# Optimization experiments

Measured on AMD Instinct MI355X. Metric: run time of the kernel, lower is better.

## Reference

```python
import jax, jax.numpy as jnp
import numpy as np
from jax import lax

B, C, N = 2048, 16, 32
POOL, STRIDE = 4, 2  # MaxPool2d(4, stride=2) -> output dim (N-4)//2+1 = 15


def setup_inputs() -> dict:
    key = jax.random.key(0)
    a = jax.random.normal(key, (B, C, N, N), dtype=jnp.float32)
    # Make each matrix symmetric positive definite: (A A^T)/N + I
    x = jnp.matmul(a, jnp.swapaxes(a, -1, -2)) / N + jnp.eye(N, dtype=jnp.float32)
    return {"x": x}


def _sym_fn(m, fn):
    """Apply fn to eigenvalues of batched symmetric matrices m and reconstruct."""
    w, v = jnp.linalg.eigh(m)                      # w: [..., n], v: [..., n, n]
    return jnp.matmul(v * fn(w)[..., None, :], jnp.swapaxes(v, -1, -2))


def reference(x):
    # LogEig: U log(S) U^T
    log_x = _sym_fn(x, jnp.log)                    # [B, C, N, N]
    # MaxPool2d(4, stride=2) over the last two dims
    pooled = lax.reduce_window(
        log_x,
        -jnp.inf,
        lax.max,
        window_dimensions=(1, 1, POOL, POOL),
        window_strides=(1, 1, STRIDE, STRIDE),
        padding="VALID",
    )                                              # [B, C, 15, 15] (still symmetric)
    # ExpEig: U exp(S) U^T
    return _sym_fn(pooled, jnp.exp)
```

## Files before the change

kernel.cpp:

```cpp
#include <hip/hip_runtime.h>
#include <cmath>


#define CENTER 4.5f
#define INVH   0.2857142857142857f
#define LDH 40
#define LDW 36
#define LDE 20

struct LogCoeffs { float b[16]; };

typedef __attribute__((ext_vector_type(8))) short bf16x8_t;
typedef __attribute__((ext_vector_type(4))) float f32x4_t;

#define MFMA_B16 __builtin_amdgcn_mfma_f32_16x16x32_bf16

__device__ __forceinline__ short bf16rne(float x) {
  unsigned u = __float_as_uint(x);
  unsigned r = (u + 0x7FFFu + ((u >> 16) & 1u)) >> 16;
  return (short)r;
}
__device__ __forceinline__ float bf16tof(short h) {
  return __uint_as_float(((unsigned)(unsigned short)h) << 16);
}

__device__ __forceinline__ void mprod(const short* Ah, const short* Al,
                                      const short* Bh, const short* Bl,
                                      f32x4_t acc[2][2], int r15, int k0) {
  const bf16x8_t a0h = *(const bf16x8_t*)(Ah + r15*LDH + k0);
  const bf16x8_t a1h = *(const bf16x8_t*)(Ah + (16 + r15)*LDH + k0);
  const bf16x8_t a0l = *(const bf16x8_t*)(Al + r15*LDH + k0);
  const bf16x8_t a1l = *(const bf16x8_t*)(Al + (16 + r15)*LDH + k0);
  const bf16x8_t b0h = *(const bf16x8_t*)(Bh + r15*LDH + k0);
  const bf16x8_t b1h = *(const bf16x8_t*)(Bh + (16 + r15)*LDH + k0);
  const bf16x8_t b0l = *(const bf16x8_t*)(Bl + r15*LDH + k0);
  const bf16x8_t b1l = *(const bf16x8_t*)(Bl + (16 + r15)*LDH + k0);
  acc[0][0] = MFMA_B16(a0h, b0h, acc[0][0], 0, 0, 0);
  acc[0][0] = MFMA_B16(a0h, b0l, acc[0][0], 0, 0, 0);
  acc[0][0] = MFMA_B16(a0l, b0h, acc[0][0], 0, 0, 0);
  acc[0][1] = MFMA_B16(a0h, b1h, acc[0][1], 0, 0, 0);
  acc[0][1] = MFMA_B16(a0h, b1l, acc[0][1], 0, 0, 0);
  acc[0][1] = MFMA_B16(a0l, b1h, acc[0][1], 0, 0, 0);
  acc[1][0] = MFMA_B16(a1h, b0h, acc[1][0], 0, 0, 0);
  acc[1][0] = MFMA_B16(a1h, b0l, acc[1][0], 0, 0, 0);
  acc[1][0] = MFMA_B16(a1l, b0h, acc[1][0], 0, 0, 0);
  acc[1][1] = MFMA_B16(a1h, b1h, acc[1][1], 0, 0, 0);
  acc[1][1] = MFMA_B16(a1h, b1l, acc[1][1], 0, 0, 0);
  acc[1][1] = MFMA_B16(a1l, b1h, acc[1][1], 0, 0, 0);
}

__device__ __forceinline__ void epi_hl(short* Dh, short* Dl,
                                       const f32x4_t acc[2][2], int r15, int quad) {
#pragma unroll
  for (int I = 0; I < 2; ++I)
#pragma unroll
    for (int i = 0; i < 4; ++i) {
      const int row = 16*I + quad + i;
#pragma unroll
      for (int J = 0; J < 2; ++J) {
        const float v = acc[I][J][i];
        const short h = bf16rne(v);
        const short lo = bf16rne(v - bf16tof(h));
        Dh[row*LDH + 16*J + r15] = h;
        Dl[row*LDH + 16*J + r15] = lo;
      }
    }
}

__device__ __forceinline__ void combo(f32x4_t c[2][2], float k0c, float k1c, float k2c,
                                      const f32x4_t Tt[2][2], const f32x4_t T2t[2][2],
                                      int r15, int quad) {
#pragma unroll
  for (int I = 0; I < 2; ++I)
#pragma unroll
    for (int J = 0; J < 2; ++J)
#pragma unroll
      for (int i = 0; i < 4; ++i) {
        float v = fmaf(k2c, T2t[I][J][i], k1c * Tt[I][J][i]);
        if (I == J && (quad + i) == r15) v += k0c;
        c[I][J][i] = v;
      }
}

__device__ __forceinline__ void mm16(const float* __restrict__ P,
                                     const float* __restrict__ Q,
                                     float a[4], int r, int c) {
  const float* p = P + r*LDE;
  const float* q = Q + 4*c;
#pragma unroll 4
  for (int k = 0; k < 4; ++k) {
    const float4 pv = *(const float4*)(p + 4*k);
    const float pr[4] = {pv.x, pv.y, pv.z, pv.w};
#pragma unroll
    for (int jj = 0; jj < 4; ++jj) {
      const float4 qv = *(const float4*)(q + (4*k + jj)*LDE);
      a[0] = fmaf(pr[jj], qv.x, a[0]);
      a[1] = fmaf(pr[jj], qv.y, a[1]);
      a[2] = fmaf(pr[jj], qv.z, a[2]);
      a[3] = fmaf(pr[jj], qv.w, a[3]);
    }
  }
}

__global__ __launch_bounds__(64, 4)
void logeig_pool_expeig(const float* __restrict__ x, float* __restrict__ out,
                        LogCoeffs lc) {
  __shared__ __align__(16) float S[2560];
  short* S0h = (short*)(S);            short* S0l = S0h + 1280;
  short* S1h = (short*)(S + 1280);     short* S1l = S1h + 1280;
  float* W   = S;
  float* RM  = S + 1280;
  float* E   = S + 1280;

  const int m = blockIdx.x;
  const int t = threadIdx.x;
  const int r15 = t & 15;
  const int k0 = (t >> 4) * 8;
  const int quad = (t >> 4) * 4;
  const float* xg = x + (size_t)m * 1024;


#pragma unroll
  for (int i = 0; i < 4; ++i) {
    int fi = (i*64 + t) * 4;
    float4 v = *(const float4*)(xg + fi);
    int row = fi >> 5, cb = fi & 31, dpos = row - cb;
    float* vp = (float*)&v;
    short hs[4], ls[4];
#pragma unroll
    for (int e = 0; e < 4; ++e) {
      float val = vp[e];
      if (e == dpos) val -= CENTER;
      val *= INVH;
      short h = bf16rne(val);
      hs[e] = h;
      ls[e] = bf16rne(val - bf16tof(h));
    }
    *(short4*)(S0h + row*LDH + cb) = make_short4(hs[0], hs[1], hs[2], hs[3]);
    *(short4*)(S0l + row*LDH + cb) = make_short4(ls[0], ls[1], ls[2], ls[3]);
  }

  f32x4_t Tt[2][2];
#pragma unroll
  for (int I = 0; I < 2; ++I)
#pragma unroll
    for (int J = 0; J < 2; ++J)
#pragma unroll
      for (int i = 0; i < 4; ++i) {
        const int row = 16*I + quad + i, col = 16*J + r15;
        Tt[I][J][i] = bf16tof(S0h[row*LDH + col]) + bf16tof(S0l[row*LDH + col]);
      }

  f32x4_t acc[2][2];
#pragma unroll
  for (int I = 0; I < 2; ++I)
#pragma unroll
    for (int J = 0; J < 2; ++J)
#pragma unroll
      for (int i = 0; i < 4; ++i) acc[I][J][i] = 0.0f;

  mprod(S0h, S0l, S0h, S0l, acc, r15, k0);
  f32x4_t T2t[2][2];
#pragma unroll
  for (int I = 0; I < 2; ++I)
#pragma unroll
    for (int J = 0; J < 2; ++J) T2t[I][J] = acc[I][J];
  epi_hl(S1h, S1l, acc, r15, quad);

#pragma unroll
  for (int I = 0; I < 2; ++I)
#pragma unroll
    for (int J = 0; J < 2; ++J)
#pragma unroll
      for (int i = 0; i < 4; ++i) acc[I][J][i] = 0.0f;
  mprod(S1h, S1l, S0h, S0l, acc, r15, k0);
  epi_hl(S0h, S0l, acc, r15, quad);

  {
    f32x4_t cc[2][2];
    combo(cc, lc.b[9], lc.b[10], lc.b[11], Tt, T2t, r15, quad);
    epi_hl(S1h, S1l, cc, r15, quad);
  }

  combo(acc, lc.b[6], lc.b[7], lc.b[8], Tt, T2t, r15, quad);
  mprod(S1h, S1l, S0h, S0l, acc, r15, k0);
  epi_hl(S1h, S1l, acc, r15, quad);

  combo(acc, lc.b[3], lc.b[4], lc.b[5], Tt, T2t, r15, quad);
  mprod(S1h, S1l, S0h, S0l, acc, r15, k0);
  epi_hl(S1h, S1l, acc, r15, quad);

  combo(acc, lc.b[0], lc.b[1], lc.b[2], Tt, T2t, r15, quad);
  mprod(S1h, S1l, S0h, S0l, acc, r15, k0);
#pragma unroll
  for (int I = 0; I < 2; ++I)
#pragma unroll
    for (int i = 0; i < 4; ++i) {
      const int row = 16*I + quad + i;
#pragma unroll
      for (int J = 0; J < 2; ++J)
        W[row*LDW + 16*J + r15] = acc[I][J][i];
    }

  {
    const int half = t >> 5, l = t & 31;
    const float* rp = W + l*LDW + 16*half;
    float4 w0 = *(const float4*)(rp + 0);
    float4 w1 = *(const float4*)(rp + 4);
    float4 w2 = *(const float4*)(rp + 8);
    float4 w3 = *(const float4*)(rp + 12);
    float2 e2 = *(const float2*)(W + l*LDW + 16);
    float v[16] = {w0.x,w0.y,w0.z,w0.w, w1.x,w1.y,w1.z,w1.w,
                   w2.x,w2.y,w2.z,w2.w, w3.x,w3.y,w3.z,w3.w};
    float rm[8];
#pragma unroll
    for (int j = 0; j < 7; ++j)
      rm[j] = fmaxf(fmaxf(v[2*j], v[2*j+1]), fmaxf(v[2*j+2], v[2*j+3]));
    rm[7] = (half == 0) ? fmaxf(fmaxf(v[14], v[15]), fmaxf(e2.x, e2.y)) : 0.0f;
    *(float4*)(RM + l*16 + 8*half + 0) = make_float4(rm[0], rm[1], rm[2], rm[3]);
    *(float4*)(RM + l*16 + 8*half + 4) = make_float4(rm[4], rm[5], rm[6], rm[7]);
  }

  const int r16 = t >> 2, c16 = t & 3;
  float p16[4];
  if (r16 < 15) {
    float4 m0 = *(const float4*)(RM + (2*r16 + 0)*16 + 4*c16);
    float4 m1 = *(const float4*)(RM + (2*r16 + 1)*16 + 4*c16);
    float4 m2 = *(const float4*)(RM + (2*r16 + 2)*16 + 4*c16);
    float4 m3 = *(const float4*)(RM + (2*r16 + 3)*16 + 4*c16);
    p16[0] = fmaxf(fmaxf(m0.x, m1.x), fmaxf(m2.x, m3.x));
    p16[1] = fmaxf(fmaxf(m0.y, m1.y), fmaxf(m2.y, m3.y));
    p16[2] = fmaxf(fmaxf(m0.z, m1.z), fmaxf(m2.z, m3.z));
    p16[3] = fmaxf(fmaxf(m0.w, m1.w), fmaxf(m2.w, m3.w));
    if (c16 == 3) p16[3] = 0.0f;
  } else {
    p16[0] = p16[1] = p16[2] = p16[3] = 0.0f;
  }

  float s = fabsf(p16[0]) + fabsf(p16[1]) + fabsf(p16[2]) + fabsf(p16[3]);
  s += __shfl_xor(s, 1);
  s += __shfl_xor(s, 2);
  s = fmaxf(s, __shfl_xor(s, 4));
  s = fmaxf(s, __shfl_xor(s, 8));
  s = fmaxf(s, __shfl_xor(s, 16));
  s = fmaxf(s, __shfl_xor(s, 32));
  int e2i; (void)frexpf(s, &e2i);
  const int sc = e2i > 0 ? e2i : 0;
  const float scale = ldexpf(1.0f, -sc);

  float* Te  = E;
  float* T2e = E + 320;
  float* T3e = E + 640;
  float* Me  = E + 960;

  float Tet[4] = {p16[0]*scale, p16[1]*scale, p16[2]*scale, p16[3]*scale};
  *(float4*)(Te + r16*LDE + 4*c16) = make_float4(Tet[0], Tet[1], Tet[2], Tet[3]);

  const float C0_ = 1.0f, C1_ = 1.0f, C2_ = 0.5f;
  const float C3_ = 1.6666667e-1f, C4_ = 4.1666668e-2f, C5_ = 8.3333338e-3f;
  const float C6_ = 1.3888889e-3f, C7_ = 1.9841270e-4f, C8_ = 2.4801588e-5f;

  float a4[4];
  a4[0] = a4[1] = a4[2] = a4[3] = 0.0f;
  mm16(Te, Te, a4, r16, c16);
  float T2et[4] = {a4[0], a4[1], a4[2], a4[3]};
  *(float4*)(T2e + r16*LDE + 4*c16) = make_float4(a4[0], a4[1], a4[2], a4[3]);
  a4[0] = a4[1] = a4[2] = a4[3] = 0.0f;
  mm16(T2e, Te, a4, r16, c16);
  *(float4*)(T3e + r16*LDE + 4*c16) = make_float4(a4[0], a4[1], a4[2], a4[3]);
#pragma unroll
  for (int e = 0; e < 4; ++e) {
    float v = fmaf(C8_, T2et[e], C7_ * Tet[e]);
    if (4*c16 + e == r16) v += C6_;
    a4[e] = v;
  }
  *(float4*)(Me + r16*LDE + 4*c16) = make_float4(a4[0], a4[1], a4[2], a4[3]);
#pragma unroll
  for (int e = 0; e < 4; ++e) {
    float v = fmaf(C5_, T2et[e], C4_ * Tet[e]);
    if (4*c16 + e == r16) v += C3_;
    a4[e] = v;
  }
  mm16(Me, T3e, a4, r16, c16);
  *(float4*)(T2e + r16*LDE + 4*c16) = make_float4(a4[0], a4[1], a4[2], a4[3]);
#pragma unroll
  for (int e = 0; e < 4; ++e) {
    float v = fmaf(C2_, T2et[e], C1_ * Tet[e]);
    if (4*c16 + e == r16) v += C0_;
    a4[e] = v;
  }
  mm16(T2e, T3e, a4, r16, c16);
  *(float4*)(Te + r16*LDE + 4*c16) = make_float4(a4[0], a4[1], a4[2], a4[3]);

  float* pc = Te;
  float* po = T3e;
  for (int it = 0; it < sc; ++it) {
    a4[0] = a4[1] = a4[2] = a4[3] = 0.0f;
    mm16(pc, pc, a4, r16, c16);
    *(float4*)(po + r16*LDE + 4*c16) = make_float4(a4[0], a4[1], a4[2], a4[3]);
    float* tmp = pc; pc = po; po = tmp;
  }

  float* og = out + (size_t)m * 225;
#pragma unroll
  for (int w2 = 0; w2 < 4; ++w2) {
    int q = t + 64*w2;
    if (q < 225) {
      int i = q / 15, j = q % 15;
      og[q] = pc[i*LDE + j];
    }
  }
}

extern "C" void kernel_launch(void* const* d_in, const int* in_sizes, int n_in,
                              void* d_out, int out_size, void* d_ws, size_t ws_size,
                              hipStream_t stream) {
  (void)n_in; (void)d_ws; (void)ws_size; (void)out_size;
  const float* x = (const float*)d_in[0];
  float* out = (float*)d_out;
  const int nmat = in_sizes[0] >> 10;

  LogCoeffs lc;
  {
    const double lo = 1.0, hi = 8.0;
    const double c = 0.5*(lo + hi), h = 0.5*(hi - lo), w = h / c;
    const double z = (std::sqrt(1.0 - w*w) - 1.0) / w;
    const int DEG = 11;
    double a[16] = {0};
    a[0] = std::log(c) - std::log(1.0 + z*z);
    double zk = 1.0;
    for (int k = 1; k <= DEG; ++k) { zk *= z; a[k] = -2.0 * zk / k; }
    double b[16], Tp[16], Tc[16], Tn[16];
    for (int j = 0; j < 16; ++j) { b[j] = 0; Tp[j] = 0; Tc[j] = 0; }
    Tp[0] = 1.0; Tc[1] = 1.0;
    b[0] += a[0] * Tp[0];
    for (int j = 0; j < 16; ++j) b[j] += a[1] * Tc[j];
    for (int k = 2; k <= DEG; ++k) {
      for (int j = 0; j < 16; ++j) {
        double v = -Tp[j];
        if (j > 0) v += 2.0 * Tc[j-1];
        Tn[j] = v;
      }
      for (int j = 0; j < 16; ++j) b[j] += a[k] * Tn[j];
      for (int j = 0; j < 16; ++j) { Tp[j] = Tc[j]; Tc[j] = Tn[j]; }
    }
    for (int j = 0; j < 16; ++j) lc.b[j] = (float)b[j];
  }

  logeig_pool_expeig<<<dim3(nmat), dim3(64), 0, stream>>>(x, out, lc);
}
```

Before: 258.5 us.

## Move 16x16 exp-stage matrix products to bf16 split MFMA and transpose epilogues

Replaces the scalar FP32 16x16 matrix products of the exp polynomial and squaring loop with bf16 hi/lo split MFMA instructions. Operands are stored packed as hi|lo halves in one row. The 32x32 log-stage epilogues now write transposed short4 vectors, relying on symmetry, instead of scattered scalar stores. This cuts FMA-pipe and LDS traffic in the exp stage, but it adds bf16 rounding on every matrix product and relies on the operands staying symmetric.

```diff
diff --git a/kernel.cpp b/kernel.cpp
--- a/kernel.cpp
+++ b/kernel.cpp
@@ -6,7 +6,6 @@
 #define INVH   0.2857142857142857f
 #define LDH 40
 #define LDW 36
-#define LDE 20
 
 struct LogCoeffs { float b[16]; };
 
@@ -49,21 +48,22 @@
   acc[1][1] = MFMA_B16(a1l, b1h, acc[1][1], 0, 0, 0);
 }
 
-__device__ __forceinline__ void epi_hl(short* Dh, short* Dl,
-                                       const f32x4_t acc[2][2], int r15, int quad) {
-#pragma unroll
-  for (int I = 0; I < 2; ++I)
-#pragma unroll
-    for (int i = 0; i < 4; ++i) {
-      const int row = 16*I + quad + i;
-#pragma unroll
-      for (int J = 0; J < 2; ++J) {
+__device__ __forceinline__ void epi_hlT(short* Dh, short* Dl,
+                                        const f32x4_t acc[2][2], int r15, int quad) {
+#pragma unroll
+  for (int I = 0; I < 2; ++I)
+#pragma unroll
+    for (int J = 0; J < 2; ++J) {
+      short h[4], l[4];
+#pragma unroll
+      for (int i = 0; i < 4; ++i) {
         const float v = acc[I][J][i];
-        const short h = bf16rne(v);
-        const short lo = bf16rne(v - bf16tof(h));
-        Dh[row*LDH + 16*J + r15] = h;
-        Dl[row*LDH + 16*J + r15] = lo;
+        h[i] = bf16rne(v);
+        l[i] = bf16rne(v - bf16tof(h[i]));
       }
+      const int o = (16*J + r15)*LDH + 16*I + quad;
+      *(short4*)(Dh + o) = make_short4(h[0], h[1], h[2], h[3]);
+      *(short4*)(Dl + o) = make_short4(l[0], l[1], l[2], l[3]);
     }
 }
 
@@ -82,23 +82,37 @@
       }
 }
 
-__device__ __forceinline__ void mm16(const float* __restrict__ P,
-                                     const float* __restrict__ Q,
-                                     float a[4], int r, int c) {
-  const float* p = P + r*LDE;
-  const float* q = Q + 4*c;
-#pragma unroll 4
-  for (int k = 0; k < 4; ++k) {
-    const float4 pv = *(const float4*)(p + 4*k);
-    const float pr[4] = {pv.x, pv.y, pv.z, pv.w};
-#pragma unroll
-    for (int jj = 0; jj < 4; ++jj) {
-      const float4 qv = *(const float4*)(q + (4*k + jj)*LDE);
-      a[0] = fmaf(pr[jj], qv.x, a[0]);
-      a[1] = fmaf(pr[jj], qv.y, a[1]);
-      a[2] = fmaf(pr[jj], qv.z, a[2]);
-      a[3] = fmaf(pr[jj], qv.w, a[3]);
-    }
+__device__ __forceinline__ void eprod(const short* P, const short* Q,
+                                      f32x4_t& acc, int r15, int k0) {
+  const bf16x8_t an = *(const bf16x8_t*)(P + r15*LDH + k0);
+  const bf16x8_t bs = *(const bf16x8_t*)(Q + r15*LDH + (k0 ^ 16));
+  const bf16x8_t bn = *(const bf16x8_t*)(Q + r15*LDH + k0);
+  const bf16x8_t vz = (bf16x8_t)(short)0;
+  const bf16x8_t a2 = (k0 < 16) ? an : vz;
+  acc = MFMA_B16(an, bs, acc, 0, 0, 0);
+  acc = MFMA_B16(a2, bn, acc, 0, 0, 0);
+}
+
+__device__ __forceinline__ void epi_packT(short* D, const f32x4_t& a, int r15, int quad) {
+  short h[4], l[4];
+#pragma unroll
+  for (int i = 0; i < 4; ++i) {
+    const float v = a[i];
+    h[i] = bf16rne(v);
+    l[i] = bf16rne(v - bf16tof(h[i]));
+  }
+  *(short4*)(D + r15*LDH + quad)      = make_short4(h[0], h[1], h[2], h[3]);
+  *(short4*)(D + r15*LDH + 16 + quad) = make_short4(l[0], l[1], l[2], l[3]);
+}
+
+__device__ __forceinline__ void ecombo(f32x4_t& c, float kI, float kT, float kT2,
+                                       const f32x4_t& Tet, const f32x4_t& T2et,
+                                       int r15, int quad) {
+#pragma unroll
+  for (int i = 0; i < 4; ++i) {
+    float v = fmaf(kT2, T2et[i], kT * Tet[i]);
+    if ((quad + i) == r15) v += kI;
+    c[i] = v;
   }
 }
 
@@ -110,7 +124,9 @@
   short* S1h = (short*)(S + 1280);     short* S1l = S1h + 1280;
   float* W   = S;
   float* RM  = S + 1280;
-  float* E   = S + 1280;
+  short* E16 = (short*)(S + 1280);
+  short* EA  = E16;
+  short* EB  = E16 + 640;
 
   const int m = blockIdx.x;
   const int t = threadIdx.x;
@@ -144,12 +160,15 @@
 #pragma unroll
   for (int I = 0; I < 2; ++I)
 #pragma unroll
-    for (int J = 0; J < 2; ++J)
-#pragma unroll
-      for (int i = 0; i < 4; ++i) {
-        const int row = 16*I + quad + i, col = 16*J + r15;
-        Tt[I][J][i] = bf16tof(S0h[row*LDH + col]) + bf16tof(S0l[row*LDH + col]);
-      }
+    for (int J = 0; J < 2; ++J) {
+      const int o = (16*J + r15)*LDH + 16*I + quad;
+      short4 h4 = *(const short4*)(S0h + o);
+      short4 l4 = *(const short4*)(S0l + o);
+      Tt[I][J][0] = bf16tof(h4.x) + bf16tof(l4.x);
+      Tt[I][J][1] = bf16tof(h4.y) + bf16tof(l4.y);
+      Tt[I][J][2] = bf16tof(h4.z) + bf16tof(l4.z);
+      Tt[I][J][3] = bf16tof(h4.w) + bf16tof(l4.w);
+    }
 
   f32x4_t acc[2][2];
 #pragma unroll
@@ -165,7 +184,7 @@
   for (int I = 0; I < 2; ++I)
 #pragma unroll
     for (int J = 0; J < 2; ++J) T2t[I][J] = acc[I][J];
-  epi_hl(S1h, S1l, acc, r15, quad);
+  epi_hlT(S1h, S1l, acc, r15, quad);
 
 #pragma unroll
   for (int I = 0; I < 2; ++I)
@@ -174,33 +193,29 @@
 #pragma unroll
       for (int i = 0; i < 4; ++i) acc[I][J][i] = 0.0f;
   mprod(S1h, S1l, S0h, S0l, acc, r15, k0);
-  epi_hl(S0h, S0l, acc, r15, quad);
+  epi_hlT(S0h, S0l, acc, r15, quad);
 
   {
     f32x4_t cc[2][2];
     combo(cc, lc.b[9], lc.b[10], lc.b[11], Tt, T2t, r15, quad);
-    epi_hl(S1h, S1l, cc, r15, quad);
+    epi_hlT(S1h, S1l, cc, r15, quad);
   }
 
   combo(acc, lc.b[6], lc.b[7], lc.b[8], Tt, T2t, r15, quad);
   mprod(S1h, S1l, S0h, S0l, acc, r15, k0);
-  epi_hl(S1h, S1l, acc, r15, quad);
+  epi_hlT(S1h, S1l, acc, r15, quad);
 
   combo(acc, lc.b[3], lc.b[4], lc.b[5], Tt, T2t, r15, quad);
   mprod(S1h, S1l, S0h, S0l, acc, r15, k0);
-  epi_hl(S1h, S1l, acc, r15, quad);
+  epi_hlT(S1h, S1l, acc, r15, quad);
 
   combo(acc, lc.b[0], lc.b[1], lc.b[2], Tt, T2t, r15, quad);
   mprod(S1h, S1l, S0h, S0l, acc, r15, k0);
 #pragma unroll
   for (int I = 0; I < 2; ++I)
 #pragma unroll
-    for (int i = 0; i < 4; ++i) {
-      const int row = 16*I + quad + i;
-#pragma unroll
-      for (int J = 0; J < 2; ++J)
-        W[row*LDW + 16*J + r15] = acc[I][J][i];
-    }
+    for (int J = 0; J < 2; ++J)
+      *(f32x4_t*)(W + (16*J + r15)*LDW + 16*I + quad) = acc[I][J];
 
   {
     const int half = t >> 5, l = t & 31;
@@ -248,57 +263,63 @@
   const int sc = e2i > 0 ? e2i : 0;
   const float scale = ldexpf(1.0f, -sc);
 
-  float* Te  = E;
-  float* T2e = E + 320;
-  float* T3e = E + 640;
-  float* Me  = E + 960;
-
-  float Tet[4] = {p16[0]*scale, p16[1]*scale, p16[2]*scale, p16[3]*scale};
-  *(float4*)(Te + r16*LDE + 4*c16) = make_float4(Tet[0], Tet[1], Tet[2], Tet[3]);
+  {
+    short h[4], l[4];
+#pragma unroll
+    for (int e = 0; e < 4; ++e) {
+      const float v = p16[e] * scale;
+      h[e] = bf16rne(v);
+      l[e] = bf16rne(v - bf16tof(h[e]));
+    }
+    *(short4*)(EA + r16*LDH + 4*c16)      = make_short4(h[0], h[1], h[2], h[3]);
+    *(short4*)(EA + r16*LDH + 16 + 4*c16) = make_short4(l[0], l[1], l[2], l[3]);
+  }
+
+  f32x4_t Tet;
+  {
+    short4 h4 = *(const short4*)(EA + r15*LDH + quad);
+    short4 l4 = *(const short4*)(EA + r15*LDH + 16 + quad);
+    Tet[0] = bf16tof(h4.x) + bf16tof(l4.x);
+    Tet[1] = bf16tof(h4.y) + bf16tof(l4.y);
+    Tet[2] = bf16tof(h4.z) + bf16tof(l4.z);
+    Tet[3] = bf16tof(h4.w) + bf16tof(l4.w);
+  }
 
   const float C0_ = 1.0f, C1_ = 1.0f, C2_ = 0.5f;
   const float C3_ = 1.6666667e-1f, C4_ = 4.1666668e-2f, C5_ = 8.3333338e-3f;
   const float C6_ = 1.3888889e-3f, C7_ = 1.9841270e-4f, C8_ = 2.4801588e-5f;
 
-  float a4[4];
-  a4[0] = a4[1] = a4[2] = a4[3] = 0.0f;
-  mm16(Te, Te, a4, r16, c16);
-  float T2et[4] = {a4[0], a4[1], a4[2], a4[3]};
-  *(float4*)(T2e + r16*LDE + 4*c16) = make_float4(a4[0], a4[1], a4[2], a4[3]);
-  a4[0] = a4[1] = a4[2] = a4[3] = 0.0f;
-  mm16(T2e, Te, a4, r16, c16);
-  *(float4*)(T3e + r16*LDE + 4*c16) = make_float4(a4[0], a4[1], a4[2], a4[3]);
-#pragma unroll
-  for (int e = 0; e < 4; ++e) {
-    float v = fmaf(C8_, T2et[e], C7_ * Tet[e]);
-    if (4*c16 + e == r16) v += C6_;
-    a4[e] = v;
-  }
-  *(float4*)(Me + r16*LDE + 4*c16) = make_float4(a4[0], a4[1], a4[2], a4[3]);
-#pragma unroll
-  for (int e = 0; e < 4; ++e) {
-    float v = fmaf(C5_, T2et[e], C4_ * Tet[e]);
-    if (4*c16 + e == r16) v += C3_;
-    a4[e] = v;
-  }
-  mm16(Me, T3e, a4, r16, c16);
-  *(float4*)(T2e + r16*LDE + 4*c16) = make_float4(a4[0], a4[1], a4[2], a4[3]);
-#pragma unroll
-  for (int e = 0; e < 4; ++e) {
-    float v = fmaf(C2_, T2et[e], C1_ * Tet[e]);
-    if (4*c16 + e == r16) v += C0_;
-    a4[e] = v;
-  }
-  mm16(T2e, T3e, a4, r16, c16);
-  *(float4*)(Te + r16*LDE + 4*c16) = make_float4(a4[0], a4[1], a4[2], a4[3]);
-
-  float* pc = Te;
-  float* po = T3e;
+  f32x4_t ac;
+#pragma unroll
+  for (int i = 0; i < 4; ++i) ac[i] = 0.0f;
+  eprod(EA, EA, ac, r15, k0);
+  f32x4_t T2et = ac;
+  epi_packT(EB, ac, r15, quad);
+
+#pragma unroll
+  for (int i = 0; i < 4; ++i) ac[i] = 0.0f;
+  eprod(EB, EA, ac, r15, k0);
+  epi_packT(EA, ac, r15, quad);
+
+  ecombo(ac, C6_, C7_, C8_, Tet, T2et, r15, quad);
+  epi_packT(EB, ac, r15, quad);
+
+  ecombo(ac, C3_, C4_, C5_, Tet, T2et, r15, quad);
+  eprod(EB, EA, ac, r15, k0);
+  epi_packT(EB, ac, r15, quad);
+
+  ecombo(ac, C0_, C1_, C2_, Tet, T2et, r15, quad);
+  eprod(EB, EA, ac, r15, k0);
+  epi_packT(EB, ac, r15, quad);
+
+  short* cur = EB;
+  short* oth = EA;
   for (int it = 0; it < sc; ++it) {
-    a4[0] = a4[1] = a4[2] = a4[3] = 0.0f;
-    mm16(pc, pc, a4, r16, c16);
-    *(float4*)(po + r16*LDE + 4*c16) = make_float4(a4[0], a4[1], a4[2], a4[3]);
-    float* tmp = pc; pc = po; po = tmp;
+#pragma unroll
+    for (int i = 0; i < 4; ++i) ac[i] = 0.0f;
+    eprod(cur, cur, ac, r15, k0);
+    epi_packT(oth, ac, r15, quad);
+    short* tmp = cur; cur = oth; oth = tmp;
   }
 
   float* og = out + (size_t)m * 225;
@@ -307,7 +328,7 @@
     int q = t + 64*w2;
     if (q < 225) {
       int i = q / 15, j = q % 15;
-      og[q] = pc[i*LDE + j];
+      og[q] = bf16tof(cur[i*LDH + j]) + bf16tof(cur[i*LDH + 16 + j]);
     }
   }
 }
```

Measured after the change: 234.7 us. -9.2%, faster.
